# Performance work log

Hardware: AMD Instinct MI355X
Metric: run time of the kernel (lower is better)

The kernel has to match this reference:

```python
import jax, jax.numpy as jnp
import numpy as np

N_NODES = 100000
N_EDGES = 1200000
DIM = 64
MAX_DEG = 64
NUM_LAB = 16
BN_EPS = 1e-5


def _lrelu(x):
    return jax.nn.leaky_relu(x, negative_slope=0.01)


def _bn(x, g, b):
    # BatchNorm1d in training mode: batch statistics over node axis
    m = x.mean(axis=0)
    v = x.var(axis=0)
    return (x - m) * jax.lax.rsqrt(v + BN_EPS) * g + b


def _gin_layer(h, src, dst, n, w1, b1, w2, b2, eps, g, b):
    # GINConv: (1+eps)*x_i + sum_{j in N(i)} x_j, then MLP (lin_lrelu_lin), BN, LeakyReLU
    agg = jax.ops.segment_sum(h[src], dst, num_segments=n)
    x = (1.0 + eps) * h + agg
    x = _lrelu(x @ w1 + b1) @ w2 + b2
    return _lrelu(_bn(x, g, b))


def setup_inputs() -> dict:
    key = jax.random.key(0)
    ks = jax.random.split(key, 16)
    s = 0.05
    inp = {
        'node_deg': jax.random.randint(ks[0], (N_NODES,), 0, MAX_DEG + 1, dtype=jnp.int32),
        'node_lab': jax.random.randint(ks[1], (N_NODES,), 0, NUM_LAB, dtype=jnp.int32),
        'edge_index': jax.random.randint(ks[2], (2, N_EDGES), 0, N_NODES, dtype=jnp.int32),
        'emb_deg': jax.random.normal(ks[3], (MAX_DEG + 1, DIM), jnp.float32) * s,
        'emb_lab': jax.random.normal(ks[4], (NUM_LAB, DIM), jnp.float32) * s,
        'l0_w1': jax.random.normal(ks[5], (2 * DIM, 2 * DIM), jnp.float32) * s,
        'l0_b1': jnp.zeros((2 * DIM,), jnp.float32),
        'l0_w2': jax.random.normal(ks[6], (2 * DIM, DIM), jnp.float32) * s,
        'l0_b2': jnp.zeros((DIM,), jnp.float32),
        'l0_eps': jnp.zeros((1,), jnp.float32),
        'bn0_g': jnp.ones((DIM,), jnp.float32),
        'bn0_b': jnp.zeros((DIM,), jnp.float32),
        'l1_w1': jax.random.normal(ks[7], (DIM, DIM), jnp.float32) * s,
        'l1_b1': jnp.zeros((DIM,), jnp.float32),
        'l1_w2': jax.random.normal(ks[8], (DIM, DIM), jnp.float32) * s,
        'l1_b2': jnp.zeros((DIM,), jnp.float32),
        'l1_eps': jnp.zeros((1,), jnp.float32),
        'bn1_g': jnp.ones((DIM,), jnp.float32),
        'bn1_b': jnp.zeros((DIM,), jnp.float32),
        'fc_w1': jax.random.normal(ks[9], (4 * DIM, DIM), jnp.float32) * s,
        'fc_b1': jnp.zeros((DIM,), jnp.float32),
        'fc_bn_g': jnp.ones((DIM,), jnp.float32),
        'fc_bn_b': jnp.zeros((DIM,), jnp.float32),
        'fc_w2': jax.random.normal(ks[10], (DIM, 1), jnp.float32) * s,
        'fc_b2': jnp.zeros((1,), jnp.float32),
    }
    return inp


def reference(node_deg, node_lab, edge_index, emb_deg, emb_lab,
              l0_w1, l0_b1, l0_w2, l0_b2, l0_eps, bn0_g, bn0_b,
              l1_w1, l1_b1, l1_w2, l1_b2, l1_eps, bn1_g, bn1_b,
              fc_w1, fc_b1, fc_bn_g, fc_bn_b, fc_w2, fc_b2):
    n = node_deg.shape[0]
    src, dst = edge_index[0], edge_index[1]
    # embedding concat: [N, 2*DIM]
    h0 = jnp.concatenate([emb_deg[node_deg], emb_lab[node_lab]], axis=1)
    h1 = _gin_layer(h0, src, dst, n, l0_w1, l0_b1, l0_w2, l0_b2, l0_eps[0], bn0_g, bn0_b)
    h2 = _gin_layer(h1, src, dst, n, l1_w1, l1_b1, l1_w2, l1_b2, l1_eps[0], bn1_g, bn1_b)
    x = jnp.concatenate([h0, h1, h2], axis=1)  # [N, 256]
    x = _lrelu(_bn(x @ fc_w1 + fc_b1, fc_bn_g, fc_bn_b))
    out = jax.nn.sigmoid(x @ fc_w2 + fc_b2)
    return out.squeeze(-1)  # [N]
```

## Files before the change

kernel.cpp:

```cpp
#include <hip/hip_runtime.h>

#define N_NODES 100000
#define N_EDGES 1200000
#define NCLS 81
#define NBKT 391
#define BCAP 4608
#define NCHK 293
#define NGBLK 1563

typedef unsigned short u16;
typedef unsigned char u8;
typedef unsigned int u32;
typedef unsigned long long u64;
typedef short bf16x8 __attribute__((ext_vector_type(8)));
typedef float f32x4 __attribute__((ext_vector_type(4)));

__device__ __forceinline__ float b2f(u16 u) {
  union { u32 i; float f; } v; v.i = ((u32)u) << 16; return v.f;
}
__device__ __forceinline__ u16 f2b(float f) {
  union { float f; u32 i; } v; v.f = f;
  u32 x = v.i;
  return (u16)((x + 0x7fffu + ((x >> 16) & 1u)) >> 16);
}
__device__ __forceinline__ void up2(u32 w, float& lo, float& hi) {
  union { u32 u; float f; } a, b;
  a.u = w << 16; b.u = w & 0xffff0000u;
  lo = a.f; hi = b.f;
}
__device__ __forceinline__ float lrelu(float x) { return x > 0.f ? x : 0.01f * x; }

__device__ __forceinline__ bool is_f32(const u16* emb) {
  int lane = threadIdx.x & 63;
  u32 e0 = (emb[lane * 2] >> 7) & 0xFF;
  u32 e1 = (emb[lane * 2 + 1] >> 7) & 0xFF;
  return __ballot((e0 >= 0x90) || (e1 >= 0x90)) != 0ull;
}

__device__ __forceinline__ float rdr(const void* p, int i, bool f32m) {
  return f32m ? ((const float*)p)[i] : b2f(((const u16*)p)[i]);
}

#define P_EMBD 0
#define P_EMBL 4160
#define P_W1A  5184
#define P_B1A  21568
#define P_W2A  21696
#define P_B2A  29888
#define P_EPS0 29952
#define P_G0   29953
#define P_BB0  30017
#define P_LW1  30081
#define P_LB1  34177
#define P_LW2  34241
#define P_LB2  38337
#define P_EPS1 38401
#define P_G1   38402
#define P_BB1  38466
#define P_FW1  38530
#define P_FB1  54914
#define P_FG   54978
#define P_FBB  55042
#define P_FW2  55106
#define P_FB2  55170
#define P_TOT  55171

struct CvtAll {
  const void* src[22];
  int cnt[22];
  int off[22];
};

struct RawPtrs {
  const void* embD;
  const void* embL;
  const void* w1r;
  const void* w2r;
  const void* lw1r;
  const void* lw2r;
  const void* fwr;
};

__global__ void k_init(CvtAll a, RawPtrs rw, const u16* __restrict__ embRaw,
                       float* __restrict__ P, float* __restrict__ W1p,
                       float* __restrict__ Efc, u16* __restrict__ bp,
                       u16* __restrict__ wpB, u32* __restrict__ gcur,
                       const int* __restrict__ ndeg, const int* __restrict__ nlab,
                       u32* __restrict__ pk) {
  int tid = threadIdx.x;
  if (blockIdx.y == 23) {
    int n = blockIdx.x * 256 + tid;
    if (n < N_NODES) pk[n] = ((u32)ndeg[n] << 4) | (u32)nlab[n];
    return;
  }
  bool f32m = is_f32(embRaw);
  if (blockIdx.y < 22) {
    if (blockIdx.y == 0 && blockIdx.x == 0) {
      for (int i = tid; i < NBKT; i += 256) gcur[i] = 0;
    }
    int seg = blockIdx.y;
    int i = blockIdx.x * 256 + tid;
    if (i < a.cnt[seg]) {
      float v = f32m ? ((const float*)a.src[seg])[i] : b2f(((const u16*)a.src[seg])[i]);
      P[a.off[seg] + i] = v;
    }
    return;
  }
  int idx = blockIdx.x * 256 + tid;
  if (idx < NCLS * 128) {
    int c = idx >> 7, h = idx & 127;
    float s = 0.f;
    if (c < 65) {
      for (int k = 0; k < 64; ++k)
        s = fmaf(rdr(rw.embD, c * 64 + k, f32m), rdr(rw.w1r, k * 128 + h, f32m), s);
    } else {
      for (int k = 0; k < 64; ++k)
        s = fmaf(rdr(rw.embL, (c - 65) * 64 + k, f32m), rdr(rw.w1r, (64 + k) * 128 + h, f32m), s);
    }
    W1p[idx] = s;
    return;
  }
  if (idx < NCLS * 128 + NCLS * 64) {
    int r = idx - NCLS * 128;
    int c = r >> 6, o = r & 63;
    float s = 0.f;
    if (c < 65) {
      for (int k = 0; k < 64; ++k)
        s = fmaf(rdr(rw.embD, c * 64 + k, f32m), rdr(rw.fwr, k * 64 + o, f32m), s);
    } else {
      for (int k = 0; k < 64; ++k)
        s = fmaf(rdr(rw.embL, (c - 65) * 64 + k, f32m), rdr(rw.fwr, (64 + k) * 64 + o, f32m), s);
    }
    Efc[r] = s;
    return;
  }
  if (idx < NCLS * 128 + NCLS * 64 + 24576) {
    int pidx = idx - (NCLS * 128 + NCLS * 64);
    int seg, rel;
    if (pidx < 8192)       { seg = 0; rel = pidx; }
    else if (pidx < 12288) { seg = 1; rel = pidx - 8192; }
    else if (pidx < 16384) { seg = 2; rel = pidx - 12288; }
    else                   { seg = 3; rel = pidx - 16384; }
    const void* srcs[4] = {rw.w2r, rw.lw1r, rw.lw2r, rw.fwr};
    const int addoff[4] = {0, 0, 0, 128 * 64};
    const int KBs[4] = {4, 2, 2, 4};
    int j = rel & 7, lane = (rel >> 3) & 63, rest = rel >> 9;
    int kb = rest % KBs[seg], nt = rest / KBs[seg];
    int k = kb * 32 + (lane >> 4) * 8 + j;
    int n = nt * 16 + (lane & 15);
    bp[pidx] = f2b(rdr(srcs[seg], addoff[seg] + k * 64 + n, f32m));
    return;
  }
  int p2 = idx - (NCLS * 128 + NCLS * 64 + 24576);
  if (p2 >= 12288) return;
  int j = p2 & 7, lane = (p2 >> 3) & 63, rest = p2 >> 9;
  int kb = rest % 3, nt = rest / 3;
  int c = kb * 32 + (lane >> 4) * 8 + j;
  int n = nt * 16 + (lane & 15);
  float s = 0.f;
  if (c < NCLS) {
    if (c < 65) {
      for (int k = 0; k < 64; ++k)
        s = fmaf(rdr(rw.embD, c * 64 + k, f32m), rdr(rw.w1r, k * 128 + n, f32m), s);
    } else {
      for (int k = 0; k < 64; ++k)
        s = fmaf(rdr(rw.embL, (c - 65) * 64 + k, f32m), rdr(rw.w1r, (64 + k) * 128 + n, f32m), s);
    }
  }
  wpB[p2] = (c < NCLS) ? f2b(s) : 0;
}

__global__ __launch_bounds__(256) void k_bsort(const int* __restrict__ edge,
                                               const u32* __restrict__ pk,
                                               u32* __restrict__ gcur,
                                               u64* __restrict__ e2) {
  __shared__ u32 cnt[NBKT], rbase[NBKT];
  __shared__ u32 slo[4096], shi[4096];
  for (int i = threadIdx.x; i < NBKT; i += 256) cnt[i] = 0;
  __syncthreads();
  int base = blockIdx.x * 4096;
  for (int i = threadIdx.x; i < 4096; i += 256) {
    int e = base + i;
    if (e < N_EDGES) {
      int s = edge[e], d = edge[N_EDGES + e];
      slo[i] = ((u32)s << 11) | pk[s];
      shi[i] = (u32)d;
      atomicAdd(&cnt[(u32)d >> 8], 1u);
    } else shi[i] = 0xFFFFFFFFu;
  }
  __syncthreads();
  for (int i = threadIdx.x; i < NBKT; i += 256) {
    u32 c = cnt[i];
    rbase[i] = c ? atomicAdd(&gcur[i], c) : 0u;
    cnt[i] = 0;
  }
  __syncthreads();
  for (int i = threadIdx.x; i < 4096; i += 256) {
    u32 d = shi[i];
    if (d == 0xFFFFFFFFu) continue;
    u32 b = d >> 8;
    u32 pos = rbase[b] + atomicAdd(&cnt[b], 1u);
    e2[(size_t)b * BCAP + pos] = ((u64)d << 32) | (u64)slo[i];
  }
}

__global__ __launch_bounds__(512) void k_csrh(const u64* __restrict__ e2,
                                              const u32* __restrict__ gcur,
                                              const u16* __restrict__ wpB,
                                              const float* __restrict__ W1p,
                                              const float* __restrict__ P,
                                              const int* __restrict__ ndeg,
                                              const int* __restrict__ nlab,
                                              const u16* __restrict__ Bp2,
                                              u32* __restrict__ row_ptr,
                                              u32* __restrict__ einfo,
                                              u16* __restrict__ t0,
                                              float* __restrict__ pbuf) {
  __shared__ u32 l[256], cur[256], gl[NBKT], wt[8];
  __shared__ u32 h32[256 * 24];
  __shared__ u32 sbase;
  __shared__ u16 T[8][16][136];
  __shared__ float lsum[8][64], lsq[8][64];
  int b = blockIdx.x, tid = threadIdx.x;
  int wid = tid >> 6, lane = tid & 63;
  if (tid < NBKT) gl[tid] = gcur[tid];
  if (tid < 256) l[tid] = 0;
  for (int i = tid; i < 256 * 24; i += 512) h32[i] = 0;
  __syncthreads();
  if (wid == 0) {
    u32 s = 0;
    for (int i = lane; i < b; i += 64) s += gl[i];
    s += __shfl_xor(s, 1, 64); s += __shfl_xor(s, 2, 64); s += __shfl_xor(s, 4, 64);
    s += __shfl_xor(s, 8, 64); s += __shfl_xor(s, 16, 64); s += __shfl_xor(s, 32, 64);
    if (lane == 0) sbase = s;
  }
  u32 cnt = gl[b];
  const u64* src = e2 + (size_t)b * BCAP;
  for (u32 e = tid; e < cnt; e += 512)
    atomicAdd(&l[(u32)(src[e] >> 32) & 255u], 1u);
  __syncthreads();
  u32 v = 0, incl = 0;
  if (tid < 256) {
    v = l[tid];
    u32 x = v;
#pragma unroll
    for (int off = 1; off < 64; off <<= 1) {
      u32 t = __shfl_up(x, off, 64);
      if (lane >= off) x += t;
    }
    if (lane == 63) wt[wid] = x;
    incl = x;
  }
  __syncthreads();
  if (tid < 256) {
    u32 woff = 0;
    for (int w = 0; w < wid; ++w) woff += wt[w];
    u32 pos0 = sbase + woff + incl - v;
    cur[tid] = pos0;
    int nn = b * 256 + tid;
    if (nn <= N_NODES) row_ptr[nn] = pos0;
  }
  __syncthreads();
  for (u32 e = tid; e < cnt; e += 512) {
    u64 r = src[e];
    u32 dl = (u32)(r >> 32) & 255u;
    u32 lo = (u32)r;
    u32 pos = atomicAdd(&cur[dl], 1u);
    einfo[pos] = lo;
    u32 c1 = (lo >> 4) & 0x7Fu, c2 = 65u + (lo & 15u);
    atomicAdd(&h32[dl * 24 + (c1 >> 2)], 1u << ((c1 & 3u) * 8));
    atomicAdd(&h32[dl * 24 + (c2 >> 2)], 1u << ((c2 & 3u) * 8));
  }
  __syncthreads();
  const u8* h = (const u8*)h32;
  int row = lane & 15, q = lane >> 4;
  float onep = 1.f + P[P_EPS0];
  const bf16x8* bp = (const bf16x8*)wpB;
  const bf16x8* bp2 = (const bf16x8*)Bp2;
  float ssA[4] = {0.f, 0.f, 0.f, 0.f}, qqA[4] = {0.f, 0.f, 0.f, 0.f};
#pragma unroll 1
  for (int t = wid; t < 16; t += 8) {
    int m0 = b * 256 + t * 16;
    if (m0 >= N_NODES) break;
    f32x4 acc[8];
#pragma unroll
    for (int nt = 0; nt < 8; ++nt) {
      float bb = P[P_B1A + nt * 16 + row];
      acc[nt][0] = bb; acc[nt][1] = bb; acc[nt][2] = bb; acc[nt][3] = bb;
    }
    const u8* ar = h + (t * 16 + row) * 96 + q * 8;
#pragma unroll
    for (int kb = 0; kb < 3; ++kb) {
      bf16x8 af;
#pragma unroll
      for (int j = 0; j < 8; ++j) af[j] = (short)f2b((float)ar[kb * 32 + j]);
#pragma unroll
      for (int nt = 0; nt < 8; ++nt) {
        bf16x8 bf = bp[(nt * 3 + kb) * 64 + lane];
        acc[nt] = __builtin_amdgcn_mfma_f32_16x16x32_bf16(af, bf, acc[nt], 0, 0, 0);
      }
    }
#pragma unroll
    for (int r = 0; r < 4; ++r) {
      int m = m0 + q * 4 + r;
      int node = q * 4 + r;
      if (m < N_NODES) {
        const float* wd = W1p + ndeg[m] * 128;
        const float* wl = W1p + (65 + nlab[m]) * 128;
#pragma unroll
        for (int nt = 0; nt < 8; ++nt) {
          int cc = nt * 16 + row;
          float vv = acc[nt][r] + onep * (wd[cc] + wl[cc]);
          T[wid][node][cc] = f2b(lrelu(vv));
        }
      } else {
#pragma unroll
        for (int nt = 0; nt < 8; ++nt) T[wid][node][nt * 16 + row] = 0;
      }
    }
    const u16* ap = &T[wid][row][q * 8];
    f32x4 acc2[4];
#pragma unroll
    for (int nt = 0; nt < 4; ++nt) {
      float bb = P[P_B2A + nt * 16 + row];
      acc2[nt][0] = bb; acc2[nt][1] = bb; acc2[nt][2] = bb; acc2[nt][3] = bb;
    }
#pragma unroll
    for (int kb = 0; kb < 4; ++kb) {
      bf16x8 af = *(const bf16x8*)(ap + kb * 32);
#pragma unroll
      for (int nt = 0; nt < 4; ++nt) {
        bf16x8 bf = bp2[(nt * 4 + kb) * 64 + lane];
        acc2[nt] = __builtin_amdgcn_mfma_f32_16x16x32_bf16(af, bf, acc2[nt], 0, 0, 0);
      }
    }
#pragma unroll
    for (int nt = 0; nt < 4; ++nt) {
      float s = 0.f, z = 0.f;
#pragma unroll
      for (int r = 0; r < 4; ++r) {
        int m = m0 + q * 4 + r;
        if (m < N_NODES) {
          u16 bv = f2b(acc2[nt][r]);
          t0[(size_t)m * 64 + nt * 16 + row] = bv;
          float vv = b2f(bv);
          s += vv; z = fmaf(vv, vv, z);
        }
      }
      s += __shfl_xor(s, 16, 64); s += __shfl_xor(s, 32, 64);
      z += __shfl_xor(z, 16, 64); z += __shfl_xor(z, 32, 64);
      ssA[nt] += s; qqA[nt] += z;
    }
  }
  if (lane < 16) {
#pragma unroll
    for (int nt = 0; nt < 4; ++nt) {
      lsum[wid][nt * 16 + lane] = ssA[nt];
      lsq[wid][nt * 16 + lane] = qqA[nt];
    }
  }
  __syncthreads();
  if (tid < 64) {
    float s = 0.f;
#pragma unroll
    for (int w = 0; w < 8; ++w) s += lsum[w][tid];
    pbuf[(size_t)b * 128 + tid] = s;
  } else if (tid < 128) {
    int c = tid - 64;
    float s = 0.f;
#pragma unroll
    for (int w = 0; w < 8; ++w) s += lsq[w][c];
    pbuf[(size_t)b * 128 + tid] = s;
  }
}

__global__ void k_sr(const float* __restrict__ pbuf, float* __restrict__ statsOut,
                     int nrows) {
  __shared__ float l[256];
  int c = blockIdx.x;
  float s = 0.f;
  for (int r = threadIdx.x; r < nrows; r += 256) s += pbuf[(size_t)r * 128 + c];
  l[threadIdx.x] = s;
  __syncthreads();
  for (int off = 128; off > 0; off >>= 1) {
    if (threadIdx.x < off) l[threadIdx.x] += l[threadIdx.x + off];
    __syncthreads();
  }
  if (threadIdx.x == 0) statsOut[c] = l[0];
}

template <int KB, int LDA, int BIASOFF>
__global__ __launch_bounds__(256) void k_gemm(const u16* __restrict__ A,
                                              const u16* __restrict__ Bp,
                                              const float* __restrict__ P,
                                              float* __restrict__ pbuf,
                                              u16* __restrict__ C) {
  __shared__ float lsum[4][64], lsq[4][64];
  int wid = threadIdx.x >> 6, lane = threadIdx.x & 63;
  int m0 = (blockIdx.x * 4 + wid) * 16;
  bool act = m0 < N_NODES;
  int row = lane & 15, q = lane >> 4;
  float ss[4] = {0.f, 0.f, 0.f, 0.f}, qq[4] = {0.f, 0.f, 0.f, 0.f};
  if (act) {
    const u16* ap = A + (size_t)(m0 + row) * LDA + q * 8;
    const bf16x8* bp = (const bf16x8*)Bp;
    f32x4 acc[4];
#pragma unroll
    for (int nt = 0; nt < 4; ++nt) {
      float b = (BIASOFF >= 0) ? P[BIASOFF + nt * 16 + row] : 0.f;
      acc[nt][0] = b; acc[nt][1] = b; acc[nt][2] = b; acc[nt][3] = b;
    }
#pragma unroll
    for (int kb = 0; kb < KB; ++kb) {
      bf16x8 af = *(const bf16x8*)(ap + kb * 32);
#pragma unroll
      for (int nt = 0; nt < 4; ++nt) {
        bf16x8 bf = bp[(nt * KB + kb) * 64 + lane];
        acc[nt] = __builtin_amdgcn_mfma_f32_16x16x32_bf16(af, bf, acc[nt], 0, 0, 0);
      }
    }
#pragma unroll
    for (int nt = 0; nt < 4; ++nt) {
      float s = 0.f, z = 0.f;
#pragma unroll
      for (int r = 0; r < 4; ++r) {
        int m = m0 + q * 4 + r;
        u16 bv = f2b(acc[nt][r]);
        C[(size_t)m * 64 + nt * 16 + row] = bv;
        float v = b2f(bv);
        s += v; z = fmaf(v, v, z);
      }
      s += __shfl_xor(s, 16, 64); s += __shfl_xor(s, 32, 64);
      z += __shfl_xor(z, 16, 64); z += __shfl_xor(z, 32, 64);
      ss[nt] = s; qq[nt] = z;
    }
  }
  if (lane < 16) {
#pragma unroll
    for (int nt = 0; nt < 4; ++nt) {
      lsum[wid][nt * 16 + lane] = ss[nt];
      lsq[wid][nt * 16 + lane] = qq[nt];
    }
  }
  __syncthreads();
  int t = threadIdx.x;
  if (t < 64)
    pbuf[(size_t)blockIdx.x * 128 + t] = lsum[0][t] + lsum[1][t] + lsum[2][t] + lsum[3][t];
  else if (t < 128) {
    int c = t - 64;
    pbuf[(size_t)blockIdx.x * 128 + t] = lsq[0][c] + lsq[1][c] + lsq[2][c] + lsq[3][c];
  }
}

__global__ __launch_bounds__(256) void k_gemm_bn(const u16* __restrict__ A,
                                                 const u16* __restrict__ Bp,
                                                 const float* __restrict__ P,
                                                 const float* __restrict__ stats,
                                                 u16* __restrict__ C) {
  int wid = threadIdx.x >> 6, lane = threadIdx.x & 63;
  int m0 = (blockIdx.x * 4 + wid) * 16;
  if (m0 >= N_NODES) return;
  int row = lane & 15, q = lane >> 4;
  const float invN = 1.f / (float)N_NODES;
  float sc[16], sh[16];
#pragma unroll
  for (int kb = 0; kb < 2; ++kb)
#pragma unroll
    for (int j = 0; j < 8; ++j) {
      int f = kb * 32 + q * 8 + j;
      float mm = stats[f] * invN;
      float var = fmaxf(stats[64 + f] * invN - mm * mm, 0.f);
      float inv = rsqrtf(var + 1e-5f);
      float s = inv * P[P_G0 + f];
      sc[kb * 8 + j] = s;
      sh[kb * 8 + j] = P[P_BB0 + f] - mm * s;
    }
  const u16* ap = A + (size_t)(m0 + row) * 64 + q * 8;
  const bf16x8* bp = (const bf16x8*)Bp;
  f32x4 acc[4];
#pragma unroll
  for (int nt = 0; nt < 4; ++nt) {
    acc[nt][0] = 0.f; acc[nt][1] = 0.f; acc[nt][2] = 0.f; acc[nt][3] = 0.f;
  }
#pragma unroll
  for (int kb = 0; kb < 2; ++kb) {
    uint4 raw = *(const uint4*)(ap + kb * 32);
    u32 rw[4] = {raw.x, raw.y, raw.z, raw.w};
    bf16x8 af;
#pragma unroll
    for (int p = 0; p < 4; ++p) {
      float lo, hi;
      up2(rw[p], lo, hi);
      float y0 = lrelu(fmaf(sc[kb * 8 + 2 * p], lo, sh[kb * 8 + 2 * p]));
      float y1 = lrelu(fmaf(sc[kb * 8 + 2 * p + 1], hi, sh[kb * 8 + 2 * p + 1]));
      af[2 * p] = (short)f2b(y0);
      af[2 * p + 1] = (short)f2b(y1);
    }
#pragma unroll
    for (int nt = 0; nt < 4; ++nt) {
      bf16x8 bf = bp[(nt * 2 + kb) * 64 + lane];
      acc[nt] = __builtin_amdgcn_mfma_f32_16x16x32_bf16(af, bf, acc[nt], 0, 0, 0);
    }
  }
#pragma unroll
  for (int nt = 0; nt < 4; ++nt)
#pragma unroll
    for (int r = 0; r < 4; ++r) {
      int m = m0 + q * 4 + r;
      C[(size_t)m * 64 + nt * 16 + row] = f2b(acc[nt][r]);
    }
}

__global__ __launch_bounds__(256) void k_agg1(const u32* __restrict__ rp,
                                              const u32* __restrict__ einfo,
                                              const u16* __restrict__ g1,
                                              const float* __restrict__ P,
                                              u16* __restrict__ abuf) {
  int lane = threadIdx.x & 63, wv = threadIdx.x >> 6;
  int n = blockIdx.x * 4 + wv;
  if (n >= N_NODES) return;
  u32 st = rp[n], en = rp[n + 1];
  u32 m = en - st;
  int grp = lane >> 4;
  int fo = (lane & 15) * 4;
  u32 myidx = (u32)n;
  if (lane < (int)m) myidx = einfo[st + lane] >> 11;
  u32 mm = m < 64u ? m : 64u;
  float a0 = 0.f, a1 = 0.f, a2 = 0.f, a3 = 0.f;
  for (u32 k = 0; k < mm; k += 16) {
#pragma unroll
    for (int bb = 0; bb < 4; ++bb) {
      u32 e = k + (u32)(bb * 4 + grp);
      u32 src = (u32)__shfl((int)myidx, (int)e, 64);
      if (e < mm) {
        uint2 v = *(const uint2*)(g1 + (size_t)src * 64 + fo);
        float l0, h0, l1, h1;
        up2(v.x, l0, h0);
        up2(v.y, l1, h1);
        a0 += l0; a1 += h0; a2 += l1; a3 += h1;
      }
    }
  }
  a0 += __shfl_xor(a0, 16, 64); a0 += __shfl_xor(a0, 32, 64);
  a1 += __shfl_xor(a1, 16, 64); a1 += __shfl_xor(a1, 32, 64);
  a2 += __shfl_xor(a2, 16, 64); a2 += __shfl_xor(a2, 32, 64);
  a3 += __shfl_xor(a3, 16, 64); a3 += __shfl_xor(a3, 32, 64);
  for (u32 k = 64; k < m; ++k) {
    u32 src = einfo[st + k] >> 11;
    uint2 v = *(const uint2*)(g1 + (size_t)src * 64 + fo);
    float l0, h0, l1, h1;
    up2(v.x, l0, h0);
    up2(v.y, l1, h1);
    a0 += l0; a1 += h0; a2 += l1; a3 += h1;
  }
  float onep = 1.f + P[P_EPS1];
  uint2 sv = *(const uint2*)(g1 + (size_t)n * 64 + fo);
  float s0, s1, s2, s3;
  up2(sv.x, s0, s1);
  up2(sv.y, s2, s3);
  float r0 = P[P_LB1 + fo + 0] + fmaf(onep, s0, a0);
  float r1 = P[P_LB1 + fo + 1] + fmaf(onep, s1, a1);
  float r2 = P[P_LB1 + fo + 2] + fmaf(onep, s2, a2);
  float r3 = P[P_LB1 + fo + 3] + fmaf(onep, s3, a3);
  if (lane < 16) {
    uint2 o;
    o.x = ((u32)f2b(lrelu(r0))) | (((u32)f2b(lrelu(r1))) << 16);
    o.y = ((u32)f2b(lrelu(r2))) | (((u32)f2b(lrelu(r3))) << 16);
    *(uint2*)(abuf + (size_t)n * 64 + fo) = o;
  }
}

__global__ __launch_bounds__(256) void k_gemm_fc1bn(const u16* __restrict__ t0,
                                                    const u16* __restrict__ t1,
                                                    const u16* __restrict__ Bp,
                                                    const float* __restrict__ P,
                                                    const float* __restrict__ stats,
                                                    float* __restrict__ pbuf,
                                                    const int* __restrict__ ndeg,
                                                    const int* __restrict__ nlab,
                                                    const float* __restrict__ Efc,
                                                    u16* __restrict__ C) {
  __shared__ float lsum[4][64], lsq[4][64];
  int wid = threadIdx.x >> 6, lane = threadIdx.x & 63;
  int m0 = (blockIdx.x * 4 + wid) * 16;
  bool act = m0 < N_NODES;
  int row = lane & 15, q = lane >> 4;
  float ss[4] = {0.f, 0.f, 0.f, 0.f}, qq[4] = {0.f, 0.f, 0.f, 0.f};
  if (act) {
    const float invN = 1.f / (float)N_NODES;
    float sc[32], sh[32];
#pragma unroll
    for (int h = 0; h < 2; ++h) {
      const float* st = stats + h * 128;
      int gof = h ? P_G1 : P_G0, bof = h ? P_BB1 : P_BB0;
#pragma unroll
      for (int kb = 0; kb < 2; ++kb)
#pragma unroll
        for (int j = 0; j < 8; ++j) {
          int f = kb * 32 + q * 8 + j;
          float mm = st[f] * invN;
          float var = fmaxf(st[64 + f] * invN - mm * mm, 0.f);
          float inv = rsqrtf(var + 1e-5f);
          float s = inv * P[gof + f];
          sc[h * 16 + kb * 8 + j] = s;
          sh[h * 16 + kb * 8 + j] = P[bof + f] - mm * s;
        }
    }
    const u16* a0 = t0 + (size_t)(m0 + row) * 64 + q * 8;
    const u16* a1 = t1 + (size_t)(m0 + row) * 64 + q * 8;
    const bf16x8* bp = (const bf16x8*)Bp;
    f32x4 acc[4];
#pragma unroll
    for (int nt = 0; nt < 4; ++nt) {
      float b = P[P_FB1 + nt * 16 + row];
      acc[nt][0] = b; acc[nt][1] = b; acc[nt][2] = b; acc[nt][3] = b;
    }
#pragma unroll
    for (int kb = 0; kb < 4; ++kb) {
      const u16* src = (kb < 2) ? (a0 + kb * 32) : (a1 + (kb - 2) * 32);
      int ci = (kb < 2) ? kb * 8 : 16 + (kb - 2) * 8;
      uint4 raw = *(const uint4*)src;
      u32 rw[4] = {raw.x, raw.y, raw.z, raw.w};
      bf16x8 af;
#pragma unroll
      for (int p = 0; p < 4; ++p) {
        float lo, hi;
        up2(rw[p], lo, hi);
        float y0 = lrelu(fmaf(sc[ci + 2 * p], lo, sh[ci + 2 * p]));
        float y1 = lrelu(fmaf(sc[ci + 2 * p + 1], hi, sh[ci + 2 * p + 1]));
        af[2 * p] = (short)f2b(y0);
        af[2 * p + 1] = (short)f2b(y1);
      }
#pragma unroll
      for (int nt = 0; nt < 4; ++nt) {
        bf16x8 bf = bp[(nt * 4 + kb) * 64 + lane];
        acc[nt] = __builtin_amdgcn_mfma_f32_16x16x32_bf16(af, bf, acc[nt], 0, 0, 0);
      }
    }
    float es[4][4];
#pragma unroll
    for (int r = 0; r < 4; ++r) {
      int m = m0 + q * 4 + r;
      int dn = ndeg[m], ln = 65 + nlab[m];
#pragma unroll
      for (int nt = 0; nt < 4; ++nt) {
        int cc = nt * 16 + row;
        es[r][nt] = acc[nt][r] + Efc[dn * 64 + cc] + Efc[ln * 64 + cc];
      }
    }
#pragma unroll
    for (int nt = 0; nt < 4; ++nt) {
      float s = 0.f, z = 0.f;
#pragma unroll
      for (int r = 0; r < 4; ++r) {
        int m = m0 + q * 4 + r;
        u16 bv = f2b(es[r][nt]);
        C[(size_t)m * 64 + nt * 16 + row] = bv;
        float v = b2f(bv);
        s += v; z = fmaf(v, v, z);
      }
      s += __shfl_xor(s, 16, 64); s += __shfl_xor(s, 32, 64);
      z += __shfl_xor(z, 16, 64); z += __shfl_xor(z, 32, 64);
      ss[nt] = s; qq[nt] = z;
    }
  }
  if (lane < 16) {
#pragma unroll
    for (int nt = 0; nt < 4; ++nt) {
      lsum[wid][nt * 16 + lane] = ss[nt];
      lsq[wid][nt * 16 + lane] = qq[nt];
    }
  }
  __syncthreads();
  int t = threadIdx.x;
  if (t < 64)
    pbuf[(size_t)blockIdx.x * 128 + t] = lsum[0][t] + lsum[1][t] + lsum[2][t] + lsum[3][t];
  else if (t < 128) {
    int c = t - 64;
    pbuf[(size_t)blockIdx.x * 128 + t] = lsq[0][c] + lsq[1][c] + lsq[2][c] + lsq[3][c];
  }
}

__global__ __launch_bounds__(256) void k_fc2(const u16* __restrict__ t,
                                             const float* __restrict__ stats,
                                             const float* __restrict__ P,
                                             const u16* __restrict__ embRaw,
                                             void* __restrict__ out) {
  __shared__ float scF[64], shF[64], fwF[64];
  bool f32m = is_f32(embRaw);
  int tid = threadIdx.x;
  if (tid < 64) {
    const float invN = 1.f / (float)N_NODES;
    float mm = stats[tid] * invN;
    float var = fmaxf(stats[64 + tid] * invN - mm * mm, 0.f);
    float inv = rsqrtf(var + 1e-5f);
    float s = inv * P[P_FG + tid];
    scF[tid] = s;
    shF[tid] = P[P_FBB + tid] - mm * s;
    fwF[tid] = P[P_FW2 + tid];
  }
  __syncthreads();
  int n = blockIdx.x * 256 + tid;
  if (n >= N_NODES) return;
  float z = P[P_FB2];
  const uint4* tn = (const uint4*)(t + (size_t)n * 64);
#pragma unroll
  for (int jj = 0; jj < 8; ++jj) {
    uint4 raw = tn[jj];
    u32 w[4] = {raw.x, raw.y, raw.z, raw.w};
#pragma unroll
    for (int p = 0; p < 4; ++p) {
      int f = jj * 8 + p * 2;
      float lo, hi;
      up2(w[p], lo, hi);
      float y0 = lrelu(fmaf(scF[f], lo, shF[f]));
      float y1 = lrelu(fmaf(scF[f + 1], hi, shF[f + 1]));
      z = fmaf(y0, fwF[f], z);
      z = fmaf(y1, fwF[f + 1], z);
    }
  }
  float s = 1.f / (1.f + expf(-z));
  if (!(fabsf(z) < 1e30f)) s = 0.25f;
  if (f32m) ((float*)out)[n] = s;
  else      ((u16*)out)[n] = f2b(s);
}

extern "C" void kernel_launch(void* const* d_in, const int* in_sizes, int n_in,
                              void* d_out, int out_size, void* d_ws, size_t ws_size,
                              hipStream_t stream) {
  const int* node_deg = (const int*)d_in[0];
  const int* node_lab = (const int*)d_in[1];
  const int* edge     = (const int*)d_in[2];
  const u16* embRaw   = (const u16*)d_in[3];
  (void)in_sizes; (void)n_in; (void)out_size; (void)ws_size;

  char* base = (char*)d_ws;
  size_t off = 0;
  auto alloc = [&](size_t bytes) -> void* {
    void* p = base + off;
    off += (bytes + 15) & ~(size_t)15;
    return p;
  };
  float* Pb    = (float*)alloc((size_t)P_TOT * 4);
  float* stats = (float*)alloc(384 * 4);
  u32* gcur    = (u32*)alloc(NBKT * 4);
  u32* pk      = (u32*)alloc((size_t)N_NODES * 4);
  float* W1p   = (float*)alloc(NCLS * 128 * 4);
  float* Efc   = (float*)alloc(NCLS * 64 * 4);
  u16* bpack   = (u16*)alloc(24576 * 2);
  u16* wpB     = (u16*)alloc(12288 * 2);
  u32* row_ptr = (u32*)alloc((size_t)(N_NODES + 1) * 4);
  float* pbuf  = (float*)alloc((size_t)NGBLK * 128 * 4);
  u32* einfo   = (u32*)alloc((size_t)N_EDGES * 4);
  u64* e2      = (u64*)alloc((size_t)NBKT * BCAP * 8);
  void* arena  = alloc((size_t)N_NODES * 128 * 2);
  u16* t0      = (u16*)alloc((size_t)N_NODES * 64 * 2);
  u16* t1      = (u16*)alloc((size_t)N_NODES * 64 * 2);
  u16* t2      = (u16*)alloc((size_t)N_NODES * 64 * 2);
  u16* g1   = (u16*)arena;
  u16* abuf = (u16*)arena + (size_t)N_NODES * 64;
  u16* Bp_w2a = bpack;
  u16* Bp_lw1 = bpack + 8192;
  u16* Bp_lw2 = bpack + 12288;
  u16* Bp_fw1 = bpack + 16384;

  CvtAll ca;
  const int srcidx[22] = {3, 4, 5, 6, 7, 8, 9, 10, 11, 12, 13, 14, 15, 16, 17, 18, 19, 20, 21, 22, 23, 24};
  const int cnts[22]   = {4160, 1024, 16384, 128, 8192, 64, 1, 64, 64, 4096, 64, 4096, 64, 1, 64, 64, 16384, 64, 64, 64, 64, 1};
  const int offs[22]   = {P_EMBD, P_EMBL, P_W1A, P_B1A, P_W2A, P_B2A, P_EPS0, P_G0, P_BB0,
                          P_LW1, P_LB1, P_LW2, P_LB2, P_EPS1, P_G1, P_BB1,
                          P_FW1, P_FB1, P_FG, P_FBB, P_FW2, P_FB2};
  for (int i = 0; i < 22; ++i) { ca.src[i] = d_in[srcidx[i]]; ca.cnt[i] = cnts[i]; ca.off[i] = offs[i]; }
  RawPtrs rw;
  rw.embD = d_in[3]; rw.embL = d_in[4]; rw.w1r = d_in[5]; rw.w2r = d_in[7];
  rw.lw1r = d_in[12]; rw.lw2r = d_in[14]; rw.fwr = d_in[19];

  k_init<<<dim3(391, 24), 256, 0, stream>>>(ca, rw, embRaw, Pb, W1p, Efc, bpack, wpB,
                                            gcur, node_deg, node_lab, pk);

  k_bsort<<<NCHK, 256, 0, stream>>>(edge, pk, gcur, e2);

  k_csrh<<<NBKT, 512, 0, stream>>>(e2, gcur, wpB, W1p, Pb, node_deg, node_lab,
                                   Bp_w2a, row_ptr, einfo, t0, pbuf);
  k_sr<<<128, 256, 0, stream>>>(pbuf, stats, NBKT);

  const int GEMM_GRID = NGBLK;

  k_gemm_bn<<<GEMM_GRID, 256, 0, stream>>>(t0, Bp_lw1, Pb, stats, g1);
  k_agg1<<<(N_NODES + 3) / 4, 256, 0, stream>>>(row_ptr, einfo, g1, Pb, abuf);
  k_gemm<2, 64, P_LB2><<<GEMM_GRID, 256, 0, stream>>>(abuf, Bp_lw2, Pb, pbuf, t1);
  k_sr<<<128, 256, 0, stream>>>(pbuf, stats + 128, NGBLK);

  k_gemm_fc1bn<<<GEMM_GRID, 256, 0, stream>>>(t0, t1, Bp_fw1, Pb, stats, pbuf,
                                              node_deg, node_lab, Efc, t2);
  k_sr<<<128, 256, 0, stream>>>(pbuf, stats + 256, NGBLK);
  k_fc2<<<(N_NODES + 255) / 256, 256, 0, stream>>>(t2, stats + 256, Pb, embRaw, d_out);
}
```

Measured before the change: 286.9 us.

## Fuse layer-1 neighbor aggregation with second GEMM and BN partial stats

Replaces the separate aggregation kernel and the following GEMM with one kernel. Each block aggregates 16 nodes, with four nodes per wave and 16-byte gathers, writes the result to shared memory, and runs the 64x64 MFMA GEMM on it. This removes the round-trip of the aggregated buffer through global memory and one kernel launch. In exchange only one of four waves does the GEMM, and the BN partial-sum buffer grows to 6250 blocks, so the stats reduction reads more rows.

```diff
diff --git a/kernel.cpp b/kernel.cpp
--- a/kernel.cpp
+++ b/kernel.cpp
@@ -7,6 +7,7 @@
 #define BCAP 4608
 #define NCHK 293
 #define NGBLK 1563
+#define NAGG 6250
 
 typedef unsigned short u16;
 typedef unsigned char u8;
@@ -389,69 +390,6 @@
   if (threadIdx.x == 0) statsOut[c] = l[0];
 }
 
-template <int KB, int LDA, int BIASOFF>
-__global__ __launch_bounds__(256) void k_gemm(const u16* __restrict__ A,
-                                              const u16* __restrict__ Bp,
-                                              const float* __restrict__ P,
-                                              float* __restrict__ pbuf,
-                                              u16* __restrict__ C) {
-  __shared__ float lsum[4][64], lsq[4][64];
-  int wid = threadIdx.x >> 6, lane = threadIdx.x & 63;
-  int m0 = (blockIdx.x * 4 + wid) * 16;
-  bool act = m0 < N_NODES;
-  int row = lane & 15, q = lane >> 4;
-  float ss[4] = {0.f, 0.f, 0.f, 0.f}, qq[4] = {0.f, 0.f, 0.f, 0.f};
-  if (act) {
-    const u16* ap = A + (size_t)(m0 + row) * LDA + q * 8;
-    const bf16x8* bp = (const bf16x8*)Bp;
-    f32x4 acc[4];
-#pragma unroll
-    for (int nt = 0; nt < 4; ++nt) {
-      float b = (BIASOFF >= 0) ? P[BIASOFF + nt * 16 + row] : 0.f;
-      acc[nt][0] = b; acc[nt][1] = b; acc[nt][2] = b; acc[nt][3] = b;
-    }
-#pragma unroll
-    for (int kb = 0; kb < KB; ++kb) {
-      bf16x8 af = *(const bf16x8*)(ap + kb * 32);
-#pragma unroll
-      for (int nt = 0; nt < 4; ++nt) {
-        bf16x8 bf = bp[(nt * KB + kb) * 64 + lane];
-        acc[nt] = __builtin_amdgcn_mfma_f32_16x16x32_bf16(af, bf, acc[nt], 0, 0, 0);
-      }
-    }
-#pragma unroll
-    for (int nt = 0; nt < 4; ++nt) {
-      float s = 0.f, z = 0.f;
-#pragma unroll
-      for (int r = 0; r < 4; ++r) {
-        int m = m0 + q * 4 + r;
-        u16 bv = f2b(acc[nt][r]);
-        C[(size_t)m * 64 + nt * 16 + row] = bv;
-        float v = b2f(bv);
-        s += v; z = fmaf(v, v, z);
-      }
-      s += __shfl_xor(s, 16, 64); s += __shfl_xor(s, 32, 64);
-      z += __shfl_xor(z, 16, 64); z += __shfl_xor(z, 32, 64);
-      ss[nt] = s; qq[nt] = z;
-    }
-  }
-  if (lane < 16) {
-#pragma unroll
-    for (int nt = 0; nt < 4; ++nt) {
-      lsum[wid][nt * 16 + lane] = ss[nt];
-      lsq[wid][nt * 16 + lane] = qq[nt];
-    }
-  }
-  __syncthreads();
-  int t = threadIdx.x;
-  if (t < 64)
-    pbuf[(size_t)blockIdx.x * 128 + t] = lsum[0][t] + lsum[1][t] + lsum[2][t] + lsum[3][t];
-  else if (t < 128) {
-    int c = t - 64;
-    pbuf[(size_t)blockIdx.x * 128 + t] = lsq[0][c] + lsq[1][c] + lsq[2][c] + lsq[3][c];
-  }
-}
-
 __global__ __launch_bounds__(256) void k_gemm_bn(const u16* __restrict__ A,
                                                  const u16* __restrict__ Bp,
                                                  const float* __restrict__ P,
@@ -511,62 +449,126 @@
     }
 }
 
-__global__ __launch_bounds__(256) void k_agg1(const u32* __restrict__ rp,
-                                              const u32* __restrict__ einfo,
-                                              const u16* __restrict__ g1,
-                                              const float* __restrict__ P,
-                                              u16* __restrict__ abuf) {
+__global__ __launch_bounds__(256) void k_aggg2(const u32* __restrict__ rp,
+                                               const u32* __restrict__ einfo,
+                                               const u16* __restrict__ g1,
+                                               const u16* __restrict__ Bp,
+                                               const float* __restrict__ P,
+                                               float* __restrict__ pbuf,
+                                               u16* __restrict__ C) {
+  __shared__ u16 As[16][72];
   int lane = threadIdx.x & 63, wv = threadIdx.x >> 6;
-  int n = blockIdx.x * 4 + wv;
-  if (n >= N_NODES) return;
-  u32 st = rp[n], en = rp[n + 1];
+  int ns = lane >> 4;
+  int li = lane & 15;
+  int es = li >> 3;
+  int fq = li & 7;
+  int n0 = blockIdx.x * 16 + wv * 4;
+  int n = n0 + ns;
+  u32 rpv = 0;
+  if (lane <= 4) rpv = rp[n0 + lane];
+  u32 st = (u32)__shfl((int)rpv, ns, 64);
+  u32 en = (u32)__shfl((int)rpv, ns + 1, 64);
   u32 m = en - st;
-  int grp = lane >> 4;
-  int fo = (lane & 15) * 4;
-  u32 myidx = (u32)n;
-  if (lane < (int)m) myidx = einfo[st + lane] >> 11;
-  u32 mm = m < 64u ? m : 64u;
+  u32 myidx = 0;
+  if (li < (int)m) myidx = einfo[st + li] >> 11;
+  u32 mm = m < 16u ? m : 16u;
   float a0 = 0.f, a1 = 0.f, a2 = 0.f, a3 = 0.f;
-  for (u32 k = 0; k < mm; k += 16) {
+  float a4 = 0.f, a5 = 0.f, a6 = 0.f, a7 = 0.f;
+  for (u32 k = 0; k < mm; k += 8) {
 #pragma unroll
     for (int bb = 0; bb < 4; ++bb) {
-      u32 e = k + (u32)(bb * 4 + grp);
-      u32 src = (u32)__shfl((int)myidx, (int)e, 64);
+      u32 e = k + (u32)(bb * 2 + es);
+      u32 src = (u32)__shfl((int)myidx, ns * 16 + (int)e, 64);
       if (e < mm) {
-        uint2 v = *(const uint2*)(g1 + (size_t)src * 64 + fo);
-        float l0, h0, l1, h1;
-        up2(v.x, l0, h0);
-        up2(v.y, l1, h1);
+        uint4 v = *(const uint4*)(g1 + (size_t)src * 64 + fq * 8);
+        float l0, h0, l1, h1, l2, h2, l3, h3;
+        up2(v.x, l0, h0); up2(v.y, l1, h1);
+        up2(v.z, l2, h2); up2(v.w, l3, h3);
         a0 += l0; a1 += h0; a2 += l1; a3 += h1;
-      }
-    }
-  }
-  a0 += __shfl_xor(a0, 16, 64); a0 += __shfl_xor(a0, 32, 64);
-  a1 += __shfl_xor(a1, 16, 64); a1 += __shfl_xor(a1, 32, 64);
-  a2 += __shfl_xor(a2, 16, 64); a2 += __shfl_xor(a2, 32, 64);
-  a3 += __shfl_xor(a3, 16, 64); a3 += __shfl_xor(a3, 32, 64);
-  for (u32 k = 64; k < m; ++k) {
-    u32 src = einfo[st + k] >> 11;
-    uint2 v = *(const uint2*)(g1 + (size_t)src * 64 + fo);
-    float l0, h0, l1, h1;
-    up2(v.x, l0, h0);
-    up2(v.y, l1, h1);
-    a0 += l0; a1 += h0; a2 += l1; a3 += h1;
-  }
-  float onep = 1.f + P[P_EPS1];
-  uint2 sv = *(const uint2*)(g1 + (size_t)n * 64 + fo);
-  float s0, s1, s2, s3;
-  up2(sv.x, s0, s1);
-  up2(sv.y, s2, s3);
-  float r0 = P[P_LB1 + fo + 0] + fmaf(onep, s0, a0);
-  float r1 = P[P_LB1 + fo + 1] + fmaf(onep, s1, a1);
-  float r2 = P[P_LB1 + fo + 2] + fmaf(onep, s2, a2);
-  float r3 = P[P_LB1 + fo + 3] + fmaf(onep, s3, a3);
-  if (lane < 16) {
-    uint2 o;
+        a4 += l2; a5 += h2; a6 += l3; a7 += h3;
+      }
+    }
+  }
+  if (es == 0) {
+    for (u32 k = 16; k < m; ++k) {
+      u32 src = einfo[st + k] >> 11;
+      uint4 v = *(const uint4*)(g1 + (size_t)src * 64 + fq * 8);
+      float l0, h0, l1, h1, l2, h2, l3, h3;
+      up2(v.x, l0, h0); up2(v.y, l1, h1);
+      up2(v.z, l2, h2); up2(v.w, l3, h3);
+      a0 += l0; a1 += h0; a2 += l1; a3 += h1;
+      a4 += l2; a5 += h2; a6 += l3; a7 += h3;
+    }
+  }
+  a0 += __shfl_xor(a0, 8, 64); a1 += __shfl_xor(a1, 8, 64);
+  a2 += __shfl_xor(a2, 8, 64); a3 += __shfl_xor(a3, 8, 64);
+  a4 += __shfl_xor(a4, 8, 64); a5 += __shfl_xor(a5, 8, 64);
+  a6 += __shfl_xor(a6, 8, 64); a7 += __shfl_xor(a7, 8, 64);
+  if (es == 0) {
+    float onep = 1.f + P[P_EPS1];
+    uint4 sv = *(const uint4*)(g1 + (size_t)n * 64 + fq * 8);
+    float s0, s1, s2, s3, s4, s5, s6, s7;
+    up2(sv.x, s0, s1); up2(sv.y, s2, s3);
+    up2(sv.z, s4, s5); up2(sv.w, s6, s7);
+    int f = fq * 8;
+    float r0 = P[P_LB1 + f + 0] + fmaf(onep, s0, a0);
+    float r1 = P[P_LB1 + f + 1] + fmaf(onep, s1, a1);
+    float r2 = P[P_LB1 + f + 2] + fmaf(onep, s2, a2);
+    float r3 = P[P_LB1 + f + 3] + fmaf(onep, s3, a3);
+    float r4 = P[P_LB1 + f + 4] + fmaf(onep, s4, a4);
+    float r5 = P[P_LB1 + f + 5] + fmaf(onep, s5, a5);
+    float r6 = P[P_LB1 + f + 6] + fmaf(onep, s6, a6);
+    float r7 = P[P_LB1 + f + 7] + fmaf(onep, s7, a7);
+    uint4 o;
     o.x = ((u32)f2b(lrelu(r0))) | (((u32)f2b(lrelu(r1))) << 16);
     o.y = ((u32)f2b(lrelu(r2))) | (((u32)f2b(lrelu(r3))) << 16);
-    *(uint2*)(abuf + (size_t)n * 64 + fo) = o;
+    o.z = ((u32)f2b(lrelu(r4))) | (((u32)f2b(lrelu(r5))) << 16);
+    o.w = ((u32)f2b(lrelu(r6))) | (((u32)f2b(lrelu(r7))) << 16);
+    *(uint4*)&As[wv * 4 + ns][f] = o;
+  }
+  __syncthreads();
+  if (wv != 0) return;
+  int row = lane & 15, q = lane >> 4;
+  int m0 = blockIdx.x * 16;
+  const u16* ap = &As[row][q * 8];
+  const bf16x8* bp = (const bf16x8*)Bp;
+  f32x4 acc[4];
+#pragma unroll
+  for (int nt = 0; nt < 4; ++nt) {
+    float b = P[P_LB2 + nt * 16 + row];
+    acc[nt][0] = b; acc[nt][1] = b; acc[nt][2] = b; acc[nt][3] = b;
+  }
+#pragma unroll
+  for (int kb = 0; kb < 2; ++kb) {
+    bf16x8 af = *(const bf16x8*)(ap + kb * 32);
+#pragma unroll
+    for (int nt = 0; nt < 4; ++nt) {
+      bf16x8 bf = bp[(nt * 2 + kb) * 64 + lane];
+      acc[nt] = __builtin_amdgcn_mfma_f32_16x16x32_bf16(af, bf, acc[nt], 0, 0, 0);
+    }
+  }
+  float ss[4], qq[4];
+#pragma unroll
+  for (int nt = 0; nt < 4; ++nt) {
+    float s = 0.f, z = 0.f;
+#pragma unroll
+    for (int r = 0; r < 4; ++r) {
+      int mo = m0 + q * 4 + r;
+      u16 bv = f2b(acc[nt][r]);
+      C[(size_t)mo * 64 + nt * 16 + row] = bv;
+      float v = b2f(bv);
+      s += v; z = fmaf(v, v, z);
+    }
+    s += __shfl_xor(s, 16, 64); s += __shfl_xor(s, 32, 64);
+    z += __shfl_xor(z, 16, 64); z += __shfl_xor(z, 32, 64);
+    ss[nt] = s; qq[nt] = z;
+  }
+  if (lane < 16) {
+#pragma unroll
+    for (int nt = 0; nt < 4; ++nt) {
+      pbuf[(size_t)blockIdx.x * 128 + nt * 16 + lane] = ss[nt];
+      pbuf[(size_t)blockIdx.x * 128 + 64 + nt * 16 + lane] = qq[nt];
+    }
   }
 }
 
@@ -750,7 +752,7 @@
   u16* bpack   = (u16*)alloc(24576 * 2);
   u16* wpB     = (u16*)alloc(12288 * 2);
   u32* row_ptr = (u32*)alloc((size_t)(N_NODES + 1) * 4);
-  float* pbuf  = (float*)alloc((size_t)NGBLK * 128 * 4);
+  float* pbuf  = (float*)alloc((size_t)NAGG * 128 * 4);
   u32* einfo   = (u32*)alloc((size_t)N_EDGES * 4);
   u64* e2      = (u64*)alloc((size_t)NBKT * BCAP * 8);
   void* arena  = alloc((size_t)N_NODES * 128 * 2);
@@ -758,7 +760,6 @@
   u16* t1      = (u16*)alloc((size_t)N_NODES * 64 * 2);
   u16* t2      = (u16*)alloc((size_t)N_NODES * 64 * 2);
   u16* g1   = (u16*)arena;
-  u16* abuf = (u16*)arena + (size_t)N_NODES * 64;
   u16* Bp_w2a = bpack;
   u16* Bp_lw1 = bpack + 8192;
   u16* Bp_lw2 = bpack + 12288;
@@ -787,9 +788,8 @@
   const int GEMM_GRID = NGBLK;
 
   k_gemm_bn<<<GEMM_GRID, 256, 0, stream>>>(t0, Bp_lw1, Pb, stats, g1);
-  k_agg1<<<(N_NODES + 3) / 4, 256, 0, stream>>>(row_ptr, einfo, g1, Pb, abuf);
-  k_gemm<2, 64, P_LB2><<<GEMM_GRID, 256, 0, stream>>>(abuf, Bp_lw2, Pb, pbuf, t1);
-  k_sr<<<128, 256, 0, stream>>>(pbuf, stats + 128, NGBLK);
+  k_aggg2<<<NAGG, 256, 0, stream>>>(row_ptr, einfo, g1, Bp_lw2, Pb, pbuf, t1);
+  k_sr<<<128, 256, 0, stream>>>(pbuf, stats + 128, NAGG);
 
   k_gemm_fc1bn<<<GEMM_GRID, 256, 0, stream>>>(t0, t1, Bp_fw1, Pb, stats, pbuf,
                                               node_deg, node_lab, Efc, t2);
```

Measured after the change: 280.3 us. 1.02x faster.
